# Optimization experiments

Hardware: AMD Instinct MI355X
Metric: run time of the kernel (lower is better)

Reference implementation:

```python
import jax, jax.numpy as jnp
import numpy as np

HEADS = 8


def setup_inputs() -> dict:
    key = jax.random.key(0)
    ks = jax.random.split(key, 5)
    B, C, H, W = 2, 256, 48, 48
    s = 0.02
    return {
        "ct": jax.random.normal(ks[0], (B, C, H, W), jnp.float32),
        "us": jax.random.normal(ks[1], (B, C, H, W), jnp.float32),
        "w_qkv_ct": jax.random.normal(ks[2], (3 * C, C), jnp.float32) * s,
        "w_qkv_us": jax.random.normal(ks[3], (3 * C, C), jnp.float32) * s,
        "w_proj": jax.random.normal(ks[4], (C, 2 * C), jnp.float32) * s,
        "b_proj": jnp.zeros((C,), jnp.float32),
    }


def _heads_view(x, B, H, W):
    # [B, C, H, W] -> [B, heads, HW, dh]
    C = x.shape[1]
    return x.reshape(B, HEADS, C // HEADS, H * W).transpose(0, 1, 3, 2)


def _cross_attn(q, k, v, scale):
    # q,k,v: [B, heads, HW, dh]
    attn = jax.nn.softmax(jnp.einsum("bhnd,bhmd->bhnm", q, k) * scale, axis=-1)
    return jnp.einsum("bhnm,bhmd->bhnd", attn, v)


def reference(ct, us, w_qkv_ct, w_qkv_us, w_proj, b_proj):
    B, C, H, W = ct.shape
    dh = C // HEADS
    scale = dh ** (-0.5)

    # 1x1 convs as channel GEMMs
    qkv1 = jnp.einsum("oc,bchw->bohw", w_qkv_ct, ct)
    qkv2 = jnp.einsum("oc,bchw->bohw", w_qkv_us, us)
    q1, k1, v1 = jnp.split(qkv1, 3, axis=1)
    q2, k2, v2 = jnp.split(qkv2, 3, axis=1)

    # CT queries attend to US keys/values
    o1 = _cross_attn(_heads_view(q1, B, H, W), _heads_view(k2, B, H, W),
                     _heads_view(v2, B, H, W), scale)
    # US queries attend to CT keys/values
    o2 = _cross_attn(_heads_view(q2, B, H, W), _heads_view(k1, B, H, W),
                     _heads_view(v1, B, H, W), scale)

    # [B, heads, HW, dh] -> [B, C, H, W]
    out1 = o1.transpose(0, 1, 3, 2).reshape(B, C, H, W)
    out2 = o2.transpose(0, 1, 3, 2).reshape(B, C, H, W)

    fused = jnp.concatenate([ct + out1, us + out2], axis=1)
    return jnp.einsum("oc,bchw->bohw", w_proj, fused) + b_proj[None, :, None, None]
```

## Files before the change

kernel.cpp:

```cpp
#include <hip/hip_runtime.h>
#include <hip/hip_bf16.h>
#include <hip/hip_cooperative_groups.h>
#include <math.h>

namespace cg = cooperative_groups;

#define HW   2304
#define CCH  256

#define QSCALE 0.25504368686637270f

typedef short short8 __attribute__((ext_vector_type(8)));
typedef float f32x4  __attribute__((ext_vector_type(4)));

__device__ inline unsigned short f2bf(float f) {
    union { float f; unsigned u; } v; v.f = f;
    unsigned r = v.u + 0x7FFF + ((v.u >> 16) & 1);
    return (unsigned short)(r >> 16);
}
__device__ inline unsigned pkbf2(float a, float b) {
    float2 f; f.x = a; f.y = b;
    union { __hip_bfloat162 h; unsigned u; } c;
    c.h = __float22bfloat162_rn(f);
    return c.u;
}
__device__ inline unsigned pktrunc(float a, float b) {
    return __builtin_amdgcn_perm(__builtin_bit_cast(unsigned, b),
                                 __builtin_bit_cast(unsigned, a), 0x07060302u);
}


__device__ __forceinline__ void prep_unit(
    int u, int t,
    const float* __restrict__ ct, const float* __restrict__ us,
    const float* __restrict__ w1, const float* __restrict__ w2,
    const float* __restrict__ w3,
    unsigned short* __restrict__ xT,
    unsigned short* __restrict__ wb1, unsigned short* __restrict__ wb2,
    unsigned short* __restrict__ w3b,
    unsigned short* __restrict__ Ts )
{
    if (u >= 576) {
        const int v_ = u - 576;
        int z, base;
        if (v_ < 192)      { z = 0; base = v_ * 1024; }
        else if (v_ < 384) { z = 1; base = (v_ - 192) * 1024; }
        else               { z = 2; base = (v_ - 384) * 1024; }
        const float* s = (z == 0) ? w1 : (z == 1) ? w2 : w3;
        unsigned short* d = (z == 0) ? wb1 : (z == 1) ? wb2 : w3b;
        const int i = base + t * 4;
        const float4 v4 = *(const float4*)&s[i];
        const float sc = (z < 2 && i < 65536) ? QSCALE : 1.f;
        uint2 p; p.x = pkbf2(v4.x * sc, v4.y * sc); p.y = pkbf2(v4.z * sc, v4.w * sc);
        *(uint2*)&d[i] = p;
        return;
    }
    const int pt = u % 36, rest = u / 36, ctile = rest & 3, z = rest >> 2;
    const float* __restrict__ src = ((z >> 1) ? us : ct) + (size_t)(z & 1) * CCH * HW;
    unsigned short* __restrict__ dst = xT + (size_t)z * HW * 256;
    const int p0 = pt * 64, c0 = ctile * 64;
    __syncthreads();
#pragma unroll
    for (int r = 0; r < 4; r++) {
        const int c = (t >> 4) + 16 * r;
        const float4 v4 = *(const float4*)&src[(size_t)(c0 + c) * HW + p0 + (t & 15) * 4];
        Ts[((t & 15) * 4 + 0) * 72 + c] = f2bf(v4.x);
        Ts[((t & 15) * 4 + 1) * 72 + c] = f2bf(v4.y);
        Ts[((t & 15) * 4 + 2) * 72 + c] = f2bf(v4.z);
        Ts[((t & 15) * 4 + 3) * 72 + c] = f2bf(v4.w);
    }
    __syncthreads();
    const int p = t >> 2, c8 = (t & 3) * 16;
    const short8 a  = *(const short8*)&Ts[p * 72 + c8];
    const short8 b8 = *(const short8*)&Ts[p * 72 + c8 + 8];
    *(short8*)&dst[(size_t)(p0 + p) * 256 + c0 + c8]     = a;
    *(short8*)&dst[(size_t)(p0 + p) * 256 + c0 + c8 + 8] = b8;
}

__device__ __forceinline__ void qkv_unit(
    int ptile, int otile, int z, int t,
    const unsigned short* __restrict__ xT,
    const unsigned short* __restrict__ wb1, const unsigned short* __restrict__ wb2,
    unsigned short* __restrict__ qkvT1, unsigned short* __restrict__ qkvT2,
    unsigned short* __restrict__ vdm1,  unsigned short* __restrict__ vdm2,
    unsigned short* __restrict__ Ws, unsigned short* __restrict__ Xs)
{
    const int inp = z >> 1, b = z & 1;
    const unsigned short* __restrict__ X = xT + (size_t)(inp * 2 + b) * HW * 256;
    const unsigned short* __restrict__ W = inp ? wb2 : wb1;
    unsigned short* __restrict__ qT = (inp ? qkvT2 : qkvT1) + (size_t)b * HW * 512;
    unsigned short* __restrict__ vd = (inp ? vdm2 : vdm1) + (size_t)b * CCH * HW;
    const int p0 = ptile * 64, o0 = otile * 64;
    const int w = t >> 6, lane = t & 63, quad = lane >> 4, m = lane & 15;
    const int sr = t >> 3, sc = t & 7;

    f32x4 acc[4] = {{0,0,0,0},{0,0,0,0},{0,0,0,0},{0,0,0,0}};
    for (int k0 = 0; k0 < 256; k0 += 64) {
        const short8 wv0 = *(const short8*)&W[(size_t)(o0 + sr) * 256 + k0 + sc * 8];
        const short8 wv1 = *(const short8*)&W[(size_t)(o0 + 32 + sr) * 256 + k0 + sc * 8];
        const short8 xv0 = *(const short8*)&X[(size_t)(p0 + sr) * 256 + k0 + sc * 8];
        const short8 xv1 = *(const short8*)&X[(size_t)(p0 + 32 + sr) * 256 + k0 + sc * 8];
        __syncthreads();
        *(short8*)&Ws[sr * 72 + sc * 8] = wv0;
        *(short8*)&Ws[(32 + sr) * 72 + sc * 8] = wv1;
        *(short8*)&Xs[sr * 72 + sc * 8] = xv0;
        *(short8*)&Xs[(32 + sr) * 72 + sc * 8] = xv1;
        __syncthreads();
#pragma unroll
        for (int kc2 = 0; kc2 < 2; kc2++) {
            const short8 af = *(const short8*)&Ws[(w * 16 + m) * 72 + kc2 * 32 + quad * 8];
#pragma unroll
            for (int pg = 0; pg < 4; pg++) {
                const short8 bf = *(const short8*)&Xs[(pg * 16 + m) * 72 + kc2 * 32 + quad * 8];
                acc[pg] = __builtin_amdgcn_mfma_f32_16x16x32_bf16(af, bf, acc[pg], 0, 0, 0);
            }
        }
    }
    __syncthreads();
    if (o0 < 512) {
#pragma unroll
        for (int pg = 0; pg < 4; pg++) {
            uint2 pk; pk.x = pkbf2(acc[pg][0], acc[pg][1]); pk.y = pkbf2(acc[pg][2], acc[pg][3]);
            *(uint2*)&Ws[(pg * 16 + m) * 72 + w * 16 + quad * 4] = pk;
        }
        __syncthreads();
        const int pr = t >> 2, cc = t & 3;
        const uint4 d0 = *(const uint4*)&Ws[pr * 72 + cc * 16];
        const uint4 d1 = *(const uint4*)&Ws[pr * 72 + cc * 16 + 8];
        *(uint4*)&qT[(size_t)(p0 + pr) * 512 + o0 + cc * 16]     = d0;
        *(uint4*)&qT[(size_t)(p0 + pr) * 512 + o0 + cc * 16 + 8] = d1;
    } else {
#pragma unroll
        for (int pg = 0; pg < 4; pg++)
#pragma unroll
            for (int r = 0; r < 4; r++)
                Ws[(w * 16 + quad * 4 + r) * 72 + pg * 16 + m] = f2bf(acc[pg][r]);
        __syncthreads();
        const int dr = t >> 2, cc = t & 3;
        const uint4 d0 = *(const uint4*)&Ws[dr * 72 + cc * 16];
        const uint4 d1 = *(const uint4*)&Ws[dr * 72 + cc * 16 + 8];
        *(uint4*)&vd[(size_t)(o0 - 512 + dr) * HW + p0 + cc * 16]     = d0;
        *(uint4*)&vd[(size_t)(o0 - 512 + dr) * HW + p0 + cc * 16 + 8] = d1;
    }
    __syncthreads();
}

__device__ __forceinline__ void attn_unit(
    int ptile, int dir, int b, int h, int t,
    const unsigned short* __restrict__ qkvT1, const unsigned short* __restrict__ qkvT2,
    const unsigned short* __restrict__ vdm1,  const unsigned short* __restrict__ vdm2,
    const float* __restrict__ ct, const float* __restrict__ us,
    unsigned short* __restrict__ fusedT,
    unsigned short* __restrict__ Ks , unsigned short* __restrict__ Vs )
{
    const unsigned short* __restrict__ Qt = (dir ? qkvT2 : qkvT1) + (size_t)b * HW * 512;
    const unsigned short* __restrict__ Kt = (dir ? qkvT1 : qkvT2) + (size_t)b * HW * 512
                                            + 256 + h * 32;
    const unsigned short* __restrict__ Vd = (dir ? vdm1 : vdm2) + ((size_t)b * CCH + h * 32) * HW;
    const float* __restrict__ src = (dir ? us : ct) + ((size_t)b * CCH + h * 32) * HW;

    const int w = t >> 6, lane = t & 63, quad = lane >> 4, m = lane & 15;
    const int kj0 = t >> 2, kcs = t & 3;
    const int pcK = kcs ^ (((kj0 >> 1) & 1) | (((kj0 >> 3) & 1) << 1));
    const int vr0 = t >> 4, vcs = t & 15;
    const int g2m = ((m >> 1) & 1) | (((m >> 2) & 1) << 1);
    const unsigned short* __restrict__ ksb =
        &Ks[((m >> 2) * 8 + (m & 3)) * 32 + (quad ^ g2m) * 8];
    const unsigned short* __restrict__ vsb = &Vs[m * 136 + quad * 8];
    const short ONE = (short)0x3F80;
    const short8 ones = {ONE,ONE,ONE,ONE,ONE,ONE,ONE,ONE};

    const int pq = ptile * 64 + w * 16 + m;
    const short8 qf = *(const short8*)&Qt[(size_t)pq * 512 + h * 32 + quad * 8];

    f32x4 acc0 = {0,0,0,0}, acc1 = {0,0,0,0}, accl = {0,0,0,0};

    for (int j0 = 0; j0 < HW; j0 += 128) {
        const short8 ka = *(const short8*)&Kt[(size_t)(j0 + kj0) * 512 + kcs * 8];
        const short8 kb = *(const short8*)&Kt[(size_t)(j0 + kj0 + 64) * 512 + kcs * 8];
        const short8 va = *(const short8*)&Vd[(size_t)vr0 * HW + j0 + vcs * 8];
        const short8 vb = *(const short8*)&Vd[(size_t)(vr0 + 16) * HW + j0 + vcs * 8];
        __syncthreads();
        *(short8*)&Ks[kj0 * 32 + pcK * 8] = ka;
        *(short8*)&Ks[(kj0 + 64) * 32 + pcK * 8] = kb;
        *(short8*)&Vs[vr0 * 136 + vcs * 8] = va;
        *(short8*)&Vs[(vr0 + 16) * 136 + vcs * 8] = vb;
        __syncthreads();

        uint4 pw4[4];
#pragma unroll
        for (int f = 0; f < 8; f++) {
            const short8 kf = *(const short8*)(ksb + ((f >> 1) * 32 + (f & 1) * 4) * 32);
            const f32x4 z = {0,0,0,0};
            const f32x4 S = __builtin_amdgcn_mfma_f32_16x16x32_bf16(kf, qf, z, 0, 0, 0);
            const float e0 = __builtin_amdgcn_exp2f(S[0]);
            const float e1 = __builtin_amdgcn_exp2f(S[1]);
            const float e2 = __builtin_amdgcn_exp2f(S[2]);
            const float e3 = __builtin_amdgcn_exp2f(S[3]);
            if ((f & 1) == 0) { pw4[f >> 1].x = pktrunc(e0, e1); pw4[f >> 1].y = pktrunc(e2, e3); }
            else              { pw4[f >> 1].z = pktrunc(e0, e1); pw4[f >> 1].w = pktrunc(e2, e3); }
        }
#pragma unroll
        for (int kt = 0; kt < 4; kt++) {
            const short8 pf = __builtin_bit_cast(short8, pw4[kt]);
            const short8 vf0 = *(const short8*)(vsb + kt * 32);
            const short8 vf1 = *(const short8*)(vsb + 16 * 136 + kt * 32);
            acc0 = __builtin_amdgcn_mfma_f32_16x16x32_bf16(vf0, pf, acc0, 0, 0, 0);
            acc1 = __builtin_amdgcn_mfma_f32_16x16x32_bf16(vf1, pf, acc1, 0, 0, 0);
            accl = __builtin_amdgcn_mfma_f32_16x16x32_bf16(ones, pf, accl, 0, 0, 0);
        }
    }

    const float inv = 1.f / accl[0];
    const int cb = dir * 256 + h * 32, d0 = quad * 4;
    unsigned short* __restrict__ fT = fusedT + ((size_t)b * HW + pq) * 512 + cb + d0;
    uint2 s0, s1;
    s0.x = pkbf2(acc0[0] * inv + src[(size_t)(d0 + 0) * HW + pq],
                 acc0[1] * inv + src[(size_t)(d0 + 1) * HW + pq]);
    s0.y = pkbf2(acc0[2] * inv + src[(size_t)(d0 + 2) * HW + pq],
                 acc0[3] * inv + src[(size_t)(d0 + 3) * HW + pq]);
    s1.x = pkbf2(acc1[0] * inv + src[(size_t)(16 + d0 + 0) * HW + pq],
                 acc1[1] * inv + src[(size_t)(16 + d0 + 1) * HW + pq]);
    s1.y = pkbf2(acc1[2] * inv + src[(size_t)(16 + d0 + 2) * HW + pq],
                 acc1[3] * inv + src[(size_t)(16 + d0 + 3) * HW + pq]);
    *(uint2*)&fT[0]  = s0;
    *(uint2*)&fT[16] = s1;
    __syncthreads();
}

__device__ __forceinline__ void proj_unit(
    int ptile, int otile, int t,
    const unsigned short* __restrict__ w3b, const unsigned short* __restrict__ fusedT,
    const float* __restrict__ bias, float* __restrict__ out,
    unsigned short* __restrict__ Ws, unsigned short* __restrict__ Xs)
{
    const int p0 = ptile * 64, o0 = otile * 64;
    const int w = t >> 6, lane = t & 63, quad = lane >> 4, m = lane & 15;
    const int sr = t >> 3, sc = t & 7;

    f32x4 acc[4] = {{0,0,0,0},{0,0,0,0},{0,0,0,0},{0,0,0,0}};
    for (int k0 = 0; k0 < 512; k0 += 64) {
        const short8 wv0 = *(const short8*)&w3b[(size_t)(o0 + sr) * 512 + k0 + sc * 8];
        const short8 wv1 = *(const short8*)&w3b[(size_t)(o0 + 32 + sr) * 512 + k0 + sc * 8];
        const short8 xv0 = *(const short8*)&fusedT[(size_t)(p0 + sr) * 512 + k0 + sc * 8];
        const short8 xv1 = *(const short8*)&fusedT[(size_t)(p0 + 32 + sr) * 512 + k0 + sc * 8];
        __syncthreads();
        *(short8*)&Ws[sr * 72 + sc * 8] = wv0;
        *(short8*)&Ws[(32 + sr) * 72 + sc * 8] = wv1;
        *(short8*)&Xs[sr * 72 + sc * 8] = xv0;
        *(short8*)&Xs[(32 + sr) * 72 + sc * 8] = xv1;
        __syncthreads();
#pragma unroll
        for (int kc2 = 0; kc2 < 2; kc2++) {
            const short8 af = *(const short8*)&Ws[(w * 16 + m) * 72 + kc2 * 32 + quad * 8];
#pragma unroll
            for (int pg = 0; pg < 4; pg++) {
                const short8 bf = *(const short8*)&Xs[(pg * 16 + m) * 72 + kc2 * 32 + quad * 8];
                acc[pg] = __builtin_amdgcn_mfma_f32_16x16x32_bf16(af, bf, acc[pg], 0, 0, 0);
            }
        }
    }
    const int b = (p0 >= HW) ? 1 : 0;
    const int pl0 = p0 - b * HW;
    float* __restrict__ ob = out + (size_t)b * CCH * HW;
    float b4[4];
#pragma unroll
    for (int r = 0; r < 4; r++) b4[r] = bias[o0 + w * 16 + quad * 4 + r];
#pragma unroll
    for (int pg = 0; pg < 4; pg++)
#pragma unroll
        for (int r = 0; r < 4; r++)
            ob[(size_t)(o0 + w * 16 + quad * 4 + r) * HW + pl0 + pg * 16 + m]
                = acc[pg][r] + b4[r];
}

__global__ __launch_bounds__(256, 5) void fused_k(
    const float* __restrict__ ct, const float* __restrict__ us,
    const float* __restrict__ w1, const float* __restrict__ w2,
    const float* __restrict__ w3, const float* __restrict__ bias,
    float* __restrict__ out,
    unsigned short* __restrict__ xT,
    unsigned short* __restrict__ wb1, unsigned short* __restrict__ wb2,
    unsigned short* __restrict__ w3b,
    unsigned short* __restrict__ qkvT1, unsigned short* __restrict__ qkvT2,
    unsigned short* __restrict__ vdm1,  unsigned short* __restrict__ vdm2,
    unsigned short* __restrict__ fusedT)
{
    cg::grid_group grid = cg::this_grid();
    __shared__ __align__(16) unsigned short smem[9216];
    const int t = threadIdx.x, nb = gridDim.x;

    for (int u = blockIdx.x; u < 1088; u += nb)
        prep_unit(u, t, ct, us, w1, w2, w3, xT, wb1, wb2, w3b, smem);
    __threadfence();
    grid.sync();

    for (int u = blockIdx.x; u < 1728; u += nb) {
        const int ptile = u % 36, rest = u / 36;
        qkv_unit(ptile, rest % 12, rest / 12, t, xT, wb1, wb2,
                 qkvT1, qkvT2, vdm1, vdm2, smem, smem + 4608);
    }
    __threadfence();
    grid.sync();

    {
        const int u = blockIdx.x;
        const int ptile = u % 36, rest = u / 36;
        attn_unit(ptile, rest >> 4, (rest >> 3) & 1, rest & 7, t,
                  qkvT1, qkvT2, vdm1, vdm2, ct, us, fusedT, smem, smem + 4096);
    }
    __threadfence();
    grid.sync();

    if (blockIdx.x < 288)
        proj_unit(blockIdx.x % 72, blockIdx.x / 72, t, w3b, fusedT, bias, out,
                  smem, smem + 4608);
}

__global__ __launch_bounds__(256, 4) void prep_k(
    const float* __restrict__ ct, const float* __restrict__ us,
    const float* __restrict__ w1, const float* __restrict__ w2,
    const float* __restrict__ w3,
    unsigned short* __restrict__ xT,
    unsigned short* __restrict__ b1, unsigned short* __restrict__ b2,
    unsigned short* __restrict__ b3)
{
    __shared__ __align__(16) unsigned short Ts[64 * 72];
    prep_unit(blockIdx.x, threadIdx.x, ct, us, w1, w2, w3, xT, b1, b2, b3, Ts);
}

__global__ __launch_bounds__(256, 4) void qkv_k(
    const unsigned short* __restrict__ xT,
    const unsigned short* __restrict__ wb1, const unsigned short* __restrict__ wb2,
    unsigned short* __restrict__ qkvT1, unsigned short* __restrict__ qkvT2,
    unsigned short* __restrict__ vdm1,  unsigned short* __restrict__ vdm2)
{
    __shared__ __align__(16) unsigned short Ws[64 * 72];
    __shared__ __align__(16) unsigned short Xs[64 * 72];
    qkv_unit(blockIdx.x, blockIdx.y, blockIdx.z, threadIdx.x,
             xT, wb1, wb2, qkvT1, qkvT2, vdm1, vdm2, Ws, Xs);
}

__global__ __launch_bounds__(256, 5) void attn_k(
    const unsigned short* __restrict__ qkvT1, const unsigned short* __restrict__ qkvT2,
    const unsigned short* __restrict__ vdm1,  const unsigned short* __restrict__ vdm2,
    const float* __restrict__ ct, const float* __restrict__ us,
    unsigned short* __restrict__ fusedT)
{
    __shared__ __align__(16) unsigned short Ks[128 * 32];
    __shared__ __align__(16) unsigned short Vs[32 * 136];
    attn_unit(blockIdx.x, blockIdx.z, blockIdx.y >> 3, blockIdx.y & 7, threadIdx.x,
              qkvT1, qkvT2, vdm1, vdm2, ct, us, fusedT, Ks, Vs);
}

__global__ __launch_bounds__(256, 4) void proj_k(
    const unsigned short* __restrict__ w3b, const unsigned short* __restrict__ fusedT,
    const float* __restrict__ bias, float* __restrict__ out)
{
    __shared__ __align__(16) unsigned short Ws[64 * 72];
    __shared__ __align__(16) unsigned short Xs[64 * 72];
    proj_unit(blockIdx.x, blockIdx.y, threadIdx.x, w3b, fusedT, bias, out, Ws, Xs);
}

extern "C" void kernel_launch(void* const* d_in, const int* in_sizes, int n_in,
                              void* d_out, int out_size, void* d_ws, size_t ws_size,
                              hipStream_t stream)
{
    const float* ct       = (const float*)d_in[0];
    const float* us       = (const float*)d_in[1];
    const float* w_qkv_ct = (const float*)d_in[2];
    const float* w_qkv_us = (const float*)d_in[3];
    const float* w_proj   = (const float*)d_in[4];
    const float* b_proj   = (const float*)d_in[5];
    float* out = (float*)d_out;

    unsigned short* wb1   = (unsigned short*)d_ws;
    unsigned short* wb2   = wb1 + (size_t)768 * 256;
    unsigned short* w3b   = wb2 + (size_t)768 * 256;
    unsigned short* xT    = w3b + (size_t)256 * 512;
    unsigned short* qkvT1 = xT    + (size_t)4 * HW * 256;
    unsigned short* qkvT2 = qkvT1 + (size_t)2 * HW * 512;
    unsigned short* vdm1  = qkvT2 + (size_t)2 * HW * 512;
    unsigned short* vdm2  = vdm1  + (size_t)2 * CCH * HW;
    unsigned short* fusedT= vdm2  + (size_t)2 * CCH * HW;

    int dev = 0, coop = 0, occ = 0;
    bool did_coop = false;
    if (hipGetDevice(&dev) == hipSuccess &&
        hipDeviceGetAttribute(&coop, hipDeviceAttributeCooperativeLaunch, dev) == hipSuccess &&
        coop &&
        hipOccupancyMaxActiveBlocksPerMultiprocessor(&occ, fused_k, 256, 0) == hipSuccess &&
        occ >= 5)
    {
        void* args[] = {
            (void*)&ct, (void*)&us, (void*)&w_qkv_ct, (void*)&w_qkv_us,
            (void*)&w_proj, (void*)&b_proj, (void*)&out,
            (void*)&xT, (void*)&wb1, (void*)&wb2, (void*)&w3b,
            (void*)&qkvT1, (void*)&qkvT2, (void*)&vdm1, (void*)&vdm2, (void*)&fusedT
        };
        did_coop = (hipLaunchCooperativeKernel((const void*)fused_k, dim3(1152), dim3(256),
                                               args, 0, stream) == hipSuccess);
    }
    if (!did_coop) {
        prep_k<<<dim3(1088), 256, 0, stream>>>(ct, us, w_qkv_ct, w_qkv_us, w_proj,
                                               xT, wb1, wb2, w3b);
        qkv_k <<<dim3(36, 12, 4), 256, 0, stream>>>(xT, wb1, wb2, qkvT1, qkvT2, vdm1, vdm2);
        attn_k<<<dim3(36, 16, 2), 256, 0, stream>>>(qkvT1, qkvT2, vdm1, vdm2, ct, us, fusedT);
        proj_k<<<dim3(72, 4), 256, 0, stream>>>(w3b, fusedT, b_proj, out);
    }
}
```

Before: 126.0 us.

## Prefetch next K-tile into registers and swizzle block-to-XCD work mapping

The qkv, attention and projection loops now issue the global loads for the next tile before the MFMA work on the current shared-memory tile, instead of loading at the top of each iteration. This is register-level double buffering meant to hide global load latency behind compute, at the cost of extra live registers. Block indices are also remapped with an (i&7)*chunk + (i>>3) swizzle so consecutive work units land on the same XCD, which is meant to improve L2 reuse of shared K/V and weight tiles.

```diff
diff --git a/kernel.cpp b/kernel.cpp
--- a/kernel.cpp
+++ b/kernel.cpp
@@ -27,6 +27,10 @@
 __device__ inline unsigned pktrunc(float a, float b) {
     return __builtin_amdgcn_perm(__builtin_bit_cast(unsigned, b),
                                  __builtin_bit_cast(unsigned, a), 0x07060302u);
+}
+
+__device__ __forceinline__ int xswz(int i, int chunk) {
+    return (i & 7) * chunk + (i >> 3);
 }
 
 
@@ -95,17 +99,26 @@
     const int sr = t >> 3, sc = t & 7;
 
     f32x4 acc[4] = {{0,0,0,0},{0,0,0,0},{0,0,0,0},{0,0,0,0}};
+
+    short8 wv0 = *(const short8*)&W[(size_t)(o0 + sr) * 256 + sc * 8];
+    short8 wv1 = *(const short8*)&W[(size_t)(o0 + 32 + sr) * 256 + sc * 8];
+    short8 xv0 = *(const short8*)&X[(size_t)(p0 + sr) * 256 + sc * 8];
+    short8 xv1 = *(const short8*)&X[(size_t)(p0 + 32 + sr) * 256 + sc * 8];
+
     for (int k0 = 0; k0 < 256; k0 += 64) {
-        const short8 wv0 = *(const short8*)&W[(size_t)(o0 + sr) * 256 + k0 + sc * 8];
-        const short8 wv1 = *(const short8*)&W[(size_t)(o0 + 32 + sr) * 256 + k0 + sc * 8];
-        const short8 xv0 = *(const short8*)&X[(size_t)(p0 + sr) * 256 + k0 + sc * 8];
-        const short8 xv1 = *(const short8*)&X[(size_t)(p0 + 32 + sr) * 256 + k0 + sc * 8];
         __syncthreads();
         *(short8*)&Ws[sr * 72 + sc * 8] = wv0;
         *(short8*)&Ws[(32 + sr) * 72 + sc * 8] = wv1;
         *(short8*)&Xs[sr * 72 + sc * 8] = xv0;
         *(short8*)&Xs[(32 + sr) * 72 + sc * 8] = xv1;
         __syncthreads();
+        const int kn = k0 + 64;
+        if (kn < 256) {
+            wv0 = *(const short8*)&W[(size_t)(o0 + sr) * 256 + kn + sc * 8];
+            wv1 = *(const short8*)&W[(size_t)(o0 + 32 + sr) * 256 + kn + sc * 8];
+            xv0 = *(const short8*)&X[(size_t)(p0 + sr) * 256 + kn + sc * 8];
+            xv1 = *(const short8*)&X[(size_t)(p0 + 32 + sr) * 256 + kn + sc * 8];
+        }
 #pragma unroll
         for (int kc2 = 0; kc2 < 2; kc2++) {
             const short8 af = *(const short8*)&Ws[(w * 16 + m) * 72 + kc2 * 32 + quad * 8];
@@ -175,17 +188,26 @@
 
     f32x4 acc0 = {0,0,0,0}, acc1 = {0,0,0,0}, accl = {0,0,0,0};
 
+    short8 ka = *(const short8*)&Kt[(size_t)kj0 * 512 + kcs * 8];
+    short8 kb = *(const short8*)&Kt[(size_t)(kj0 + 64) * 512 + kcs * 8];
+    short8 va = *(const short8*)&Vd[(size_t)vr0 * HW + vcs * 8];
+    short8 vb = *(const short8*)&Vd[(size_t)(vr0 + 16) * HW + vcs * 8];
+
     for (int j0 = 0; j0 < HW; j0 += 128) {
-        const short8 ka = *(const short8*)&Kt[(size_t)(j0 + kj0) * 512 + kcs * 8];
-        const short8 kb = *(const short8*)&Kt[(size_t)(j0 + kj0 + 64) * 512 + kcs * 8];
-        const short8 va = *(const short8*)&Vd[(size_t)vr0 * HW + j0 + vcs * 8];
-        const short8 vb = *(const short8*)&Vd[(size_t)(vr0 + 16) * HW + j0 + vcs * 8];
         __syncthreads();
         *(short8*)&Ks[kj0 * 32 + pcK * 8] = ka;
         *(short8*)&Ks[(kj0 + 64) * 32 + pcK * 8] = kb;
         *(short8*)&Vs[vr0 * 136 + vcs * 8] = va;
         *(short8*)&Vs[(vr0 + 16) * 136 + vcs * 8] = vb;
         __syncthreads();
+
+        const int jn = j0 + 128;
+        if (jn < HW) {
+            ka = *(const short8*)&Kt[(size_t)(jn + kj0) * 512 + kcs * 8];
+            kb = *(const short8*)&Kt[(size_t)(jn + kj0 + 64) * 512 + kcs * 8];
+            va = *(const short8*)&Vd[(size_t)vr0 * HW + jn + vcs * 8];
+            vb = *(const short8*)&Vd[(size_t)(vr0 + 16) * HW + jn + vcs * 8];
+        }
 
         uint4 pw4[4];
 #pragma unroll
@@ -239,17 +261,26 @@
     const int sr = t >> 3, sc = t & 7;
 
     f32x4 acc[4] = {{0,0,0,0},{0,0,0,0},{0,0,0,0},{0,0,0,0}};
+
+    short8 wv0 = *(const short8*)&w3b[(size_t)(o0 + sr) * 512 + sc * 8];
+    short8 wv1 = *(const short8*)&w3b[(size_t)(o0 + 32 + sr) * 512 + sc * 8];
+    short8 xv0 = *(const short8*)&fusedT[(size_t)(p0 + sr) * 512 + sc * 8];
+    short8 xv1 = *(const short8*)&fusedT[(size_t)(p0 + 32 + sr) * 512 + sc * 8];
+
     for (int k0 = 0; k0 < 512; k0 += 64) {
-        const short8 wv0 = *(const short8*)&w3b[(size_t)(o0 + sr) * 512 + k0 + sc * 8];
-        const short8 wv1 = *(const short8*)&w3b[(size_t)(o0 + 32 + sr) * 512 + k0 + sc * 8];
-        const short8 xv0 = *(const short8*)&fusedT[(size_t)(p0 + sr) * 512 + k0 + sc * 8];
-        const short8 xv1 = *(const short8*)&fusedT[(size_t)(p0 + 32 + sr) * 512 + k0 + sc * 8];
         __syncthreads();
         *(short8*)&Ws[sr * 72 + sc * 8] = wv0;
         *(short8*)&Ws[(32 + sr) * 72 + sc * 8] = wv1;
         *(short8*)&Xs[sr * 72 + sc * 8] = xv0;
         *(short8*)&Xs[(32 + sr) * 72 + sc * 8] = xv1;
         __syncthreads();
+        const int kn = k0 + 64;
+        if (kn < 512) {
+            wv0 = *(const short8*)&w3b[(size_t)(o0 + sr) * 512 + kn + sc * 8];
+            wv1 = *(const short8*)&w3b[(size_t)(o0 + 32 + sr) * 512 + kn + sc * 8];
+            xv0 = *(const short8*)&fusedT[(size_t)(p0 + sr) * 512 + kn + sc * 8];
+            xv1 = *(const short8*)&fusedT[(size_t)(p0 + 32 + sr) * 512 + kn + sc * 8];
+        }
 #pragma unroll
         for (int kc2 = 0; kc2 < 2; kc2++) {
             const short8 af = *(const short8*)&Ws[(w * 16 + m) * 72 + kc2 * 32 + quad * 8];
@@ -295,7 +326,8 @@
     __threadfence();
     grid.sync();
 
-    for (int u = blockIdx.x; u < 1728; u += nb) {
+    for (int i = blockIdx.x; i < 1728; i += nb) {
+        const int u = xswz(i, 216);
         const int ptile = u % 36, rest = u / 36;
         qkv_unit(ptile, rest % 12, rest / 12, t, xT, wb1, wb2,
                  qkvT1, qkvT2, vdm1, vdm2, smem, smem + 4608);
@@ -304,7 +336,7 @@
     grid.sync();
 
     {
-        const int u = blockIdx.x;
+        const int u = xswz(blockIdx.x, 144);
         const int ptile = u % 36, rest = u / 36;
         attn_unit(ptile, rest >> 4, (rest >> 3) & 1, rest & 7, t,
                   qkvT1, qkvT2, vdm1, vdm2, ct, us, fusedT, smem, smem + 4096);
@@ -312,9 +344,11 @@
     __threadfence();
     grid.sync();
 
-    if (blockIdx.x < 288)
-        proj_unit(blockIdx.x % 72, blockIdx.x / 72, t, w3b, fusedT, bias, out,
+    if (blockIdx.x < 288) {
+        const int u = xswz(blockIdx.x, 36);
+        proj_unit(u % 72, u / 72, t, w3b, fusedT, bias, out,
                   smem, smem + 4608);
+    }
 }
 
 __global__ __launch_bounds__(256, 4) void prep_k(
```

Result: no change. 126.0 us (-0.0%).
